# Kernel tuning notes

Measured on AMD Instinct MI355X. Metric: run time of the kernel, lower is better.

The kernel has to match this reference:

```python
import jax, jax.numpy as jnp
import numpy as np

B, T, C, H = 128, 200, 171, 1024  # batch, timesteps, frame_dim, hidden


def setup_inputs() -> dict:
    key = jax.random.key(0)
    ks = jax.random.split(key, 16)
    s = 1.0 / np.sqrt(H)  # PyTorch default init range for LSTMCell/Linear

    def u(k, shape):
        return jax.random.uniform(k, shape, jnp.float32, -s, s)

    inp = {
        "seq": jax.random.normal(ks[0], (B, T, C), jnp.float32),
        # LSTMCell 1: input C -> hidden H
        "W_ih1": u(ks[1], (4 * H, C)), "W_hh1": u(ks[2], (4 * H, H)),
        "b_ih1": u(ks[3], (4 * H,)),   "b_hh1": u(ks[4], (4 * H,)),
        # LSTMCell 2: H -> H
        "W_ih2": u(ks[5], (4 * H, H)), "W_hh2": u(ks[6], (4 * H, H)),
        "b_ih2": u(ks[7], (4 * H,)),   "b_hh2": u(ks[8], (4 * H,)),
        # LSTMCell 3: H -> H
        "W_ih3": u(ks[9], (4 * H, H)), "W_hh3": u(ks[10], (4 * H, H)),
        "b_ih3": u(ks[11], (4 * H,)),  "b_hh3": u(ks[12], (4 * H,)),
        # decoder Linear: H -> C
        "W_dec": u(ks[13], (C, H)), "b_dec": u(ks[14], (C,)),
        "cond": 5, "gt": 5,
    }
    return inp


def _lstm_cell(x, h, c, W_ih, W_hh, b_ih, b_hh):
    # PyTorch LSTMCell gate order: i, f, g, o
    gates = x @ W_ih.T + b_ih + h @ W_hh.T + b_hh
    i, f, g, o = jnp.split(gates, 4, axis=-1)
    c_new = jax.nn.sigmoid(f) * c + jax.nn.sigmoid(i) * jnp.tanh(g)
    h_new = jax.nn.sigmoid(o) * jnp.tanh(c_new)
    return h_new, c_new


def reference(seq, W_ih1, W_hh1, b_ih1, b_hh1,
              W_ih2, W_hh2, b_ih2, b_hh2,
              W_ih3, W_hh3, b_ih3, b_hh3,
              W_dec, b_dec, cond, gt):
    Bb, Tt, Cc = seq.shape
    Hh = W_hh1.shape[1]
    # Static teacher-forcing pattern: gt ground-truth steps, then cond self-conditioned steps.
    pattern = jnp.asarray(np.array(([True] * gt + [False] * cond) * 100, dtype=bool)[:Tt])

    def step(carry, xs):
        h1, c1, h2, c2, h3, c3, xo = carry
        x_t, use_gt = xs
        x = jnp.where(use_gt, x_t, xo)
        h1, c1 = _lstm_cell(x, h1, c1, W_ih1, W_hh1, b_ih1, b_hh1)
        h2, c2 = _lstm_cell(h1, h2, c2, W_ih2, W_hh2, b_ih2, b_hh2)
        h3, c3 = _lstm_cell(h2, h3, c3, W_ih3, W_hh3, b_ih3, b_hh3)
        xo = h3 @ W_dec.T + b_dec
        return (h1, c1, h2, c2, h3, c3, xo), xo

    z = jnp.zeros((Bb, Hh), seq.dtype)
    init = (z, z, z, z, z, z, jnp.zeros((Bb, Cc), seq.dtype))
    _, out = jax.lax.scan(step, init, (seq.transpose(1, 0, 2), pattern))
    return out.transpose(1, 0, 2)  # [B, T, C]
```

## Files before the change

kernel.cpp:

```cpp
#include <hip/hip_runtime.h>

#define TT 200
#define BB 128
#define CC 171
#define HH 1024

typedef __attribute__((ext_vector_type(8))) short short8;
typedef __attribute__((ext_vector_type(4))) float f32x4;

__device__ __forceinline__ unsigned short f2bf(float f) {
  unsigned int u = __float_as_uint(f);
  u += 0x7fff + ((u >> 16) & 1);
  return (unsigned short)(u >> 16);
}
__device__ __forceinline__ float sigmoidf_(float x) { return 1.f / (1.f + __expf(-x)); }

__device__ __forceinline__ int4 ld_coh16(const void* p) {
  int4 r;
  asm volatile("global_load_dwordx4 %0, %1, off sc0 sc1" : "=v"(r) : "v"(p));
  return r;
}
__device__ __forceinline__ void st_coh2(void* p, unsigned int v) {
  asm volatile("global_store_short %0, %1, off sc0 sc1" :: "v"(p), "v"(v) : "memory");
}
__device__ __forceinline__ void drain_vm() {
  asm volatile("s_waitcnt vmcnt(0)" ::: "memory");
}
__device__ __forceinline__ void wait4() {
  asm volatile("s_waitcnt vmcnt(4)" ::: "memory");
}
__device__ __forceinline__ void bar_lds() {
  asm volatile("s_waitcnt lgkmcnt(0)" ::: "memory");
  __builtin_amdgcn_s_barrier();
  asm volatile("" ::: "memory");
}

__device__ __forceinline__ void groupbar(int* B, int tid, int epoch) {
  __builtin_amdgcn_s_barrier();
  if (tid == 0) {
    if (__hip_atomic_fetch_add(&B[0], 1, __ATOMIC_RELAXED, __HIP_MEMORY_SCOPE_AGENT) == epoch * 64 - 1)
      __hip_atomic_store(&B[32], epoch, __ATOMIC_RELAXED, __HIP_MEMORY_SCOPE_AGENT);
    while (__hip_atomic_load(&B[32], __ATOMIC_RELAXED, __HIP_MEMORY_SCOPE_AGENT) < epoch)
      __builtin_amdgcn_s_sleep(1);
  }
  asm volatile("" ::: "memory");
  __builtin_amdgcn_s_barrier();
  asm volatile("" ::: "memory");
}

struct Pre4 { int4 v[4]; };
struct Pre5 { int4 v[5]; };

__device__ __forceinline__ void prefetch_old(const unsigned short* A2, int sA2,
    int m0, int grp, int row, int lj, Pre4& P) {
  const unsigned short* base = A2 + (size_t)(m0 + row) * sA2 + ((lj ^ (row & 7)) << 3);
#pragma unroll
  for (int j = 0; j < 4; ++j)
    P.v[j] = ld_coh16(base + (grp * 4 + j) * 64);
}

__device__ __forceinline__ void prefetch_gtl1(const float* seqt,
    const unsigned short* H1old, int m0, int grp, int row, int lj, Pre5& P) {
  const int kt0 = grp * 5;
  const int ktn = 4 + (grp < 3 ? 1 : 0);
  const float* srow = seqt + (size_t)(m0 + row) * (TT * CC);
  const unsigned short* hbase = H1old + (size_t)(m0 + row) * HH + ((lj ^ (row & 7)) << 3);
#pragma unroll
  for (int i = 0; i < 5; ++i) {
    if (i < ktn) {
      int kt = kt0 + i;
      if (kt < 3) {
        int c0 = kt * 64 + ((lj ^ (row & 7)) << 3);
        unsigned int w[4];
#pragma unroll
        for (int jj = 0; jj < 4; ++jj) {
          int ca = c0 + 2 * jj, cb = c0 + 2 * jj + 1;
          float va = (ca < CC) ? srow[ca] : 0.f;
          float vb = (cb < CC) ? srow[cb] : 0.f;
          w[jj] = (unsigned int)f2bf(va) | ((unsigned int)f2bf(vb) << 16);
        }
        P.v[i] = make_int4(w[0], w[1], w[2], w[3]);
      } else {
        P.v[i] = ld_coh16(hbase + (kt - 3) * 64);
      }
    }
  }
  drain_vm();
}

__device__ __forceinline__ void exchange_cell(f32x4 acc0, f32x4 acc1,
    const float* bias, float& creg, unsigned short* Hout,
    char* smem, int m0, int n0, int ntile, int tid) {
  const int wave = tid >> 6, lane = tid & 63;
  const int grp = wave >> 2, gw = wave & 3;
  const int fl = lane & 15, fh = lane >> 4;
  bar_lds();
  float* ex = (float*)smem;
#pragma unroll
  for (int r = 0; r < 4; ++r) {
    ex[((grp * 4 + gw) * 32 + fh * 4 + r) * 16 + fl] = acc0[r];
    ex[((grp * 4 + gw) * 32 + 16 + fh * 4 + r) * 16 + fl] = acc1[r];
  }
  bar_lds();
  if (tid < 512) {
    int urow = tid >> 4, uu = tid & 15;
    float g4[4];
#pragma unroll
    for (int gg = 0; gg < 4; ++gg) {
      float s = ex[(gg * 32 + urow) * 16 + uu] + ex[((4 + gg) * 32 + urow) * 16 + uu]
              + ex[((8 + gg) * 32 + urow) * 16 + uu] + ex[((12 + gg) * 32 + urow) * 16 + uu];
      g4[gg] = s + bias[n0 + gg * 16 + uu];
    }
    float cn = sigmoidf_(g4[1]) * creg + sigmoidf_(g4[0]) * tanhf(g4[2]);
    creg = cn;
    st_coh2(Hout + (size_t)(m0 + urow) * HH + ntile * 16 + uu,
            (unsigned int)f2bf(sigmoidf_(g4[3]) * tanhf(cn)));
  }
}

__device__ __forceinline__ void lstm_split(
    const unsigned short* __restrict__ A1, int sA1,
    const unsigned short* __restrict__ Wa, int sWa,
    const unsigned short* __restrict__ Wb, int sWb,
    const float* __restrict__ bias,
    float& creg, unsigned short* __restrict__ Hout,
    char* smem, int m0, int n0, int ntile, int tid, const Pre4& P)
{
  const int wave = tid >> 6, lane = tid & 63;
  const int grp = wave >> 2, gw = wave & 3;
  const int lrow = lane >> 3, lj = lane & 7;
  const int fl = lane & 15, fh = lane >> 4;
  const int row = gw * 8 + lrow;
  const int swz = (fl & 7) << 4;
  const int wrowi = n0 + gw * 16 + fl;
  char* G = smem + grp * 32768;

  int4 anew[4];
  const unsigned short* nbase = A1 + (size_t)(m0 + row) * sA1 + ((lj ^ (row & 7)) << 3);
#pragma unroll
  for (int j = 0; j < 4; ++j)
    anew[j] = ld_coh16(nbase + (grp * 4 + j) * 64);
  wait4();
#pragma unroll
  for (int j = 0; j < 4; ++j)
    *(int4*)(G + (4 + j) * 4096 + row * 128 + lj * 16) = P.v[j];
  bar_lds();

  f32x4 acc0 = {0.f, 0.f, 0.f, 0.f}, acc1 = {0.f, 0.f, 0.f, 0.f};
  const unsigned short* wbr = Wb + (size_t)wrowi * sWb + fh * 8;
#pragma unroll
  for (int j = 0; j < 4; ++j) {
#pragma unroll
    for (int kk = 0; kk < 2; ++kk) {
      short8 b0 = *(const short8*)(wbr + (grp * 4 + j) * 64 + kk * 32);
      int colb = kk * 64 + fh * 16;
      short8 a0 = *(const short8*)(G + (4 + j) * 4096 + fl * 128 + (colb ^ swz));
      short8 a1 = *(const short8*)(G + (4 + j) * 4096 + (16 + fl) * 128 + (colb ^ swz));
      acc0 = __builtin_amdgcn_mfma_f32_16x16x32_bf16(a0, b0, acc0, 0, 0, 0);
      acc1 = __builtin_amdgcn_mfma_f32_16x16x32_bf16(a1, b0, acc1, 0, 0, 0);
    }
  }
  drain_vm();
#pragma unroll
  for (int j = 0; j < 4; ++j)
    *(int4*)(G + j * 4096 + row * 128 + lj * 16) = anew[j];
  bar_lds();
  const unsigned short* war = Wa + (size_t)wrowi * sWa + fh * 8;
#pragma unroll
  for (int j = 0; j < 4; ++j) {
#pragma unroll
    for (int kk = 0; kk < 2; ++kk) {
      short8 b0 = *(const short8*)(war + (grp * 4 + j) * 64 + kk * 32);
      int colb = kk * 64 + fh * 16;
      short8 a0 = *(const short8*)(G + j * 4096 + fl * 128 + (colb ^ swz));
      short8 a1 = *(const short8*)(G + j * 4096 + (16 + fl) * 128 + (colb ^ swz));
      acc0 = __builtin_amdgcn_mfma_f32_16x16x32_bf16(a0, b0, acc0, 0, 0, 0);
      acc1 = __builtin_amdgcn_mfma_f32_16x16x32_bf16(a1, b0, acc1, 0, 0, 0);
    }
  }
  exchange_cell(acc0, acc1, bias, creg, Hout, smem, m0, n0, ntile, tid);
}

__device__ __forceinline__ void lstm_gtl1(const Pre5& P,
    const unsigned short* __restrict__ Wih1p, const unsigned short* __restrict__ Whh1,
    const float* __restrict__ bias,
    float& creg, unsigned short* __restrict__ Hout,
    char* smem, int m0, int n0, int ntile, int tid)
{
  const int wave = tid >> 6, lane = tid & 63;
  const int grp = wave >> 2, gw = wave & 3;
  const int lrow = lane >> 3, lj = lane & 7;
  const int fl = lane & 15, fh = lane >> 4;
  const int row = gw * 8 + lrow;
  const int swz = (fl & 7) << 4;
  const int wrowi = n0 + gw * 16 + fl;
  const int kt0 = grp * 5;
  const int ktn = 4 + (grp < 3 ? 1 : 0);
  char* G = smem + grp * 32768;

#pragma unroll
  for (int i = 0; i < 5; ++i)
    if (i < ktn) *(int4*)(G + i * 4096 + row * 128 + lj * 16) = P.v[i];
  bar_lds();

  f32x4 acc0 = {0.f, 0.f, 0.f, 0.f}, acc1 = {0.f, 0.f, 0.f, 0.f};
#pragma unroll
  for (int i = 0; i < 5; ++i) {
    if (i < ktn) {
      int kt = kt0 + i;
      const unsigned short* wr = (kt < 3)
          ? Wih1p + (size_t)wrowi * 192 + kt * 64 + fh * 8
          : Whh1 + (size_t)wrowi * HH + (kt - 3) * 64 + fh * 8;
#pragma unroll
      for (int kk = 0; kk < 2; ++kk) {
        short8 b0 = *(const short8*)(wr + kk * 32);
        int colb = kk * 64 + fh * 16;
        short8 a0 = *(const short8*)(G + i * 4096 + fl * 128 + (colb ^ swz));
        short8 a1 = *(const short8*)(G + i * 4096 + (16 + fl) * 128 + (colb ^ swz));
        acc0 = __builtin_amdgcn_mfma_f32_16x16x32_bf16(a0, b0, acc0, 0, 0, 0);
        acc1 = __builtin_amdgcn_mfma_f32_16x16x32_bf16(a1, b0, acc1, 0, 0, 0);
      }
    }
  }
  exchange_cell(acc0, acc1, bias, creg, Hout, smem, m0, n0, ntile, tid);
}

__device__ __forceinline__ void dec_out(
    const unsigned short* __restrict__ H3in, const unsigned short* __restrict__ Wd,
    const float* __restrict__ bd, float* __restrict__ out,
    int t, char* smem, int d, int tid, int m0)
{
  const int wave = tid >> 6, lane = tid & 63;
  const int lrow = lane >> 3, lj = lane & 7;
  const int fl = lane & 15, fh = lane >> 4;
  const int n0 = d * 16;
  char* Dr = smem + 65536 + wave * 4096;
  int4 r4[4];
#pragma unroll
  for (int j = 0; j < 4; ++j) {
    int row = j * 8 + lrow;
    r4[j] = ld_coh16(H3in + (size_t)(m0 + row) * HH + wave * 64 + ((lj ^ (row & 7)) << 3));
  }
  drain_vm();
#pragma unroll
  for (int j = 0; j < 4; ++j) {
    int row = j * 8 + lrow;
    *(int4*)(Dr + row * 128 + lj * 16) = r4[j];
  }
  f32x4 acc0 = {0.f, 0.f, 0.f, 0.f}, acc1 = {0.f, 0.f, 0.f, 0.f};
  const unsigned short* Wrow = Wd + (size_t)(n0 + fl) * HH + wave * 64 + fh * 8;
  const int swz = (fl & 7) << 4;
#pragma unroll
  for (int kk = 0; kk < 2; ++kk) {
    short8 b0 = *(const short8*)(Wrow + kk * 32);
    int colb = kk * 64 + fh * 16;
    short8 a0 = *(const short8*)(Dr + fl * 128 + (colb ^ swz));
    short8 a1 = *(const short8*)(Dr + (16 + fl) * 128 + (colb ^ swz));
    acc0 = __builtin_amdgcn_mfma_f32_16x16x32_bf16(a0, b0, acc0, 0, 0, 0);
    acc1 = __builtin_amdgcn_mfma_f32_16x16x32_bf16(a1, b0, acc1, 0, 0, 0);
  }
  float* pex = (float*)(smem + 32768);
#pragma unroll
  for (int r = 0; r < 4; ++r) {
    pex[(wave * 32 + fh * 4 + r) * 16 + fl] = acc0[r];
    pex[(wave * 32 + 16 + fh * 4 + r) * 16 + fl] = acc1[r];
  }
  bar_lds();
  if (tid < 512) {
    int rrow = tid >> 4, uu = tid & 15;
    int c = n0 + uu;
    if (c < CC) {
      float s = 0.f;
#pragma unroll
      for (int v = 0; v < 16; ++v) s += pex[(v * 32 + rrow) * 16 + uu];
      out[(size_t)(m0 + rrow) * (TT * CC) + (size_t)t * CC + c] = s + bd[c];
    }
  }
}

__global__ __launch_bounds__(1024, 4) void persistent_lstm(
    const unsigned short* __restrict__ Wih1p, const unsigned short* __restrict__ Whh1,
    const unsigned short* __restrict__ Wf, const unsigned short* __restrict__ W2,
    const unsigned short* __restrict__ W3, const unsigned short* __restrict__ Wd,
    const float* __restrict__ B1gt, const float* __restrict__ B1sc,
    const float* __restrict__ B2, const float* __restrict__ B3, const float* __restrict__ Bd,
    unsigned short* __restrict__ Hb, const float* __restrict__ seq, float* __restrict__ out,
    const int* __restrict__ gtp, const int* __restrict__ condp, int* __restrict__ bar)
{
  __shared__ char smem[131072];
  const int wg = blockIdx.x, tid = threadIdx.x;
  const int xg = wg & 7, sl = wg >> 3;
  const int ntile = xg * 8 + (sl >> 2);
  const int mgrp = sl & 3;
  const int m0 = mgrp * 32;
  const int n0 = ntile * 64;
  const int gt = *gtp, cond = *condp;
  const int per = gt + cond;
  const int lane = tid & 63, wave = tid >> 6;
  const int grp = wave >> 2, gw = wave & 3;
  const int lrow = lane >> 3, lj = lane & 7;
  const int row = gw * 8 + lrow;

  int dd = ((ntile & 7) << 3) | (ntile >> 3);
  const int decid = (dd < 11) ? dd : -1;

  unsigned short* H1[2] = { Hb + 0 * BB * HH, Hb + 1 * BB * HH };
  unsigned short* H2[2] = { Hb + 2 * BB * HH, Hb + 3 * BB * HH };
  unsigned short* H3[2] = { Hb + 4 * BB * HH, Hb + 5 * BB * HH };
  int* B = bar + mgrp * 256;

  float c1 = 0.f, c2 = 0.f, c3 = 0.f;
  Pre4 aold; Pre5 a1pre;
  int e = 0, tm = 0;
  bool gts = (per > 0) ? (0 < gt) : true;
  if (gts) prefetch_gtl1(seq, H1[0], m0, grp, row, lj, a1pre);
  else     prefetch_old(H1[0], HH, m0, grp, row, lj, aold);

  for (int t = 0; t < TT; ++t) {
    int p = t & 1;
    if (gts) lstm_gtl1(a1pre, Wih1p, Whh1, B1gt, c1, H1[1 - p], smem, m0, n0, ntile, tid);
    else     lstm_split(H3[p], HH, Wf, HH, Whh1, HH, B1sc, c1, H1[1 - p],
                        smem, m0, n0, ntile, tid, aold);
    if (decid >= 0 && t > 0) dec_out(H3[p], Wd, Bd, out, t - 1, smem, decid, tid, m0);
    prefetch_old(H2[p], HH, m0, grp, row, lj, aold);
    wait4();
    groupbar(B, tid, ++e);
    lstm_split(H1[1 - p], HH, W2, 2048, W2 + 1024, 2048, B2, c2, H2[1 - p],
               smem, m0, n0, ntile, tid, aold);
    prefetch_old(H3[p], HH, m0, grp, row, lj, aold);
    wait4();
    groupbar(B, tid, ++e);
    lstm_split(H2[1 - p], HH, W3, 2048, W3 + 1024, 2048, B3, c3, H3[1 - p],
               smem, m0, n0, ntile, tid, aold);
    int tmn = (tm + 1 == per) ? 0 : tm + 1;
    bool gtsn = (per > 0) ? (tmn < gt) : true;
    if (t + 1 < TT) {
      if (gtsn) prefetch_gtl1(seq + (size_t)(t + 1) * CC, H1[1 - p], m0, grp, row, lj, a1pre);
      else { prefetch_old(H1[1 - p], HH, m0, grp, row, lj, aold); wait4(); }
    } else drain_vm();
    groupbar(B, tid, ++e);
    tm = tmn; gts = gtsn;
  }
  if (decid >= 0) dec_out(H3[0], Wd, Bd, out, TT - 1, smem, decid, tid, m0);
}

__device__ __forceinline__ int perm_orig_row(int np) {
  return ((np >> 4) & 3) * HH + ((np >> 6) << 4) + (np & 15);
}

__global__ void conv_wih1p(const float* __restrict__ Wih, unsigned short* __restrict__ dst) {
  int np = blockIdx.x, k = threadIdx.x;
  int n = perm_orig_row(np);
  dst[(size_t)np * 192 + k] = f2bf((k < CC) ? Wih[(size_t)n * CC + k] : 0.f);
}

__global__ void conv_whh1(const float* __restrict__ Whh, unsigned short* __restrict__ dst) {
  int np = blockIdx.y, k = blockIdx.x * 256 + threadIdx.x;
  int n = perm_orig_row(np);
  dst[(size_t)np * HH + k] = f2bf(Whh[(size_t)n * HH + k]);
}

__global__ void conv_w23(const float* __restrict__ Wih, const float* __restrict__ Whh,
                         unsigned short* __restrict__ dst) {
  int k = blockIdx.x * 256 + threadIdx.x;
  int np = blockIdx.y;
  int n = perm_orig_row(np);
  float v = (k < HH) ? Wih[(size_t)n * HH + k] : Whh[(size_t)n * HH + (k - HH)];
  dst[(size_t)np * 2048 + k] = f2bf(v);
}

__global__ void conv_wd(const float* __restrict__ Wsrc, unsigned short* __restrict__ dst) {
  int k = blockIdx.x * 256 + threadIdx.x;
  int row = blockIdx.y;
  dst[(size_t)row * HH + k] = f2bf((row < CC) ? Wsrc[(size_t)row * HH + k] : 0.f);
}

__global__ void wf_gemm(const float* __restrict__ Wih1, const float* __restrict__ Wdec,
                        unsigned short* __restrict__ Wfo) {
  int j = blockIdx.x * 256 + threadIdx.x;
  int np = blockIdx.y;
  int n = perm_orig_row(np);
  const float* wr = Wih1 + (size_t)n * CC;
  float acc = 0.f;
  for (int c = 0; c < CC; ++c) acc = fmaf(wr[c], Wdec[(size_t)c * HH + j], acc);
  Wfo[(size_t)np * HH + j] = f2bf(acc);
}

__global__ void bias_all(const float* bi1, const float* bh1, const float* Wih1, const float* bdec,
                         const float* bi2, const float* bh2, const float* bi3, const float* bh3,
                         float* o1gt, float* o1sc, float* o2, float* o3, float* od) {
  int idx = blockIdx.x * 256 + threadIdx.x;
  if (idx < 4096) {
    int n = perm_orig_row(idx);
    float b = bi1[n] + bh1[n];
    o1gt[idx] = b;
    const float* wr = Wih1 + (size_t)n * CC;
    float acc = 0.f;
    for (int c = 0; c < CC; ++c) acc = fmaf(wr[c], bdec[c], acc);
    o1sc[idx] = b + acc;
  } else if (idx < 8192) {
    int np = idx - 4096; int n = perm_orig_row(np);
    o2[np] = bi2[n] + bh2[n];
  } else if (idx < 12288) {
    int np = idx - 8192; int n = perm_orig_row(np);
    o3[np] = bi3[n] + bh3[n];
  } else if (idx < 12464) {
    int c2 = idx - 12288;
    od[c2] = (c2 < CC) ? bdec[c2] : 0.f;
  }
}

__global__ void init_state(unsigned short* __restrict__ Hall, int* __restrict__ bar) {
  int idx = blockIdx.x * blockDim.x + threadIdx.x;
  if (idx < 6 * BB * HH) Hall[idx] = 0;
  if (idx < 1024) bar[idx] = 0;
}

extern "C" void kernel_launch(void* const* d_in, const int* in_sizes, int n_in,
                              void* d_out, int out_size, void* d_ws, size_t ws_size,
                              hipStream_t stream)
{
  const float* seq   = (const float*)d_in[0];
  const float* W_ih1 = (const float*)d_in[1];
  const float* W_hh1 = (const float*)d_in[2];
  const float* b_ih1 = (const float*)d_in[3];
  const float* b_hh1 = (const float*)d_in[4];
  const float* W_ih2 = (const float*)d_in[5];
  const float* W_hh2 = (const float*)d_in[6];
  const float* b_ih2 = (const float*)d_in[7];
  const float* b_hh2 = (const float*)d_in[8];
  const float* W_ih3 = (const float*)d_in[9];
  const float* W_hh3 = (const float*)d_in[10];
  const float* b_ih3 = (const float*)d_in[11];
  const float* b_hh3 = (const float*)d_in[12];
  const float* W_dec = (const float*)d_in[13];
  const float* b_dec = (const float*)d_in[14];
  const int* condp   = (const int*)d_in[15];
  const int* gtp     = (const int*)d_in[16];
  float* out = (float*)d_out;
  char* ws = (char*)d_ws;

  if (ws_size < 53908480) return;

  unsigned short* Wih1p = (unsigned short*)(ws + 0);
  unsigned short* Whh1  = (unsigned short*)(ws + 1572864);
  unsigned short* Wf    = (unsigned short*)(ws + 9961472);
  unsigned short* W2    = (unsigned short*)(ws + 18350080);
  unsigned short* W3    = (unsigned short*)(ws + 35127296);
  unsigned short* Wd    = (unsigned short*)(ws + 51904512);
  float* B1gt = (float*)(ws + 52264960);
  float* B1sc = (float*)(ws + 52281344);
  float* B2   = (float*)(ws + 52297728);
  float* B3   = (float*)(ws + 52314112);
  float* Bd   = (float*)(ws + 52330496);
  unsigned short* Hbase = (unsigned short*)(ws + 52331520);
  int* bar = (int*)(ws + 53904384);

  conv_wih1p<<<dim3(4096),    192, 0, stream>>>(W_ih1, Wih1p);
  conv_whh1 <<<dim3(4, 4096), 256, 0, stream>>>(W_hh1, Whh1);
  wf_gemm   <<<dim3(4, 4096), 256, 0, stream>>>(W_ih1, W_dec, Wf);
  conv_w23  <<<dim3(8, 4096), 256, 0, stream>>>(W_ih2, W_hh2, W2);
  conv_w23  <<<dim3(8, 4096), 256, 0, stream>>>(W_ih3, W_hh3, W3);
  conv_wd   <<<dim3(4, 176),  256, 0, stream>>>(W_dec, Wd);
  bias_all  <<<dim3(49),      256, 0, stream>>>(b_ih1, b_hh1, W_ih1, b_dec,
                                                b_ih2, b_hh2, b_ih3, b_hh3,
                                                B1gt, B1sc, B2, B3, Bd);
  init_state<<<dim3(3072),    256, 0, stream>>>(Hbase, bar);

  persistent_lstm<<<dim3(256), dim3(1024), 0, stream>>>(
      Wih1p, Whh1, Wf, W2, W3, Wd, B1gt, B1sc, B2, B3, Bd,
      Hbase, seq, out, gtp, condp, bar);
}
```

Baseline: 7.139 ms.

## Split persistent LSTM into 512 workgroups of 512 threads with 16-row batch tiles

The persistent kernel moves from 256 workgroups of 1024 threads (32 batch rows each) to 512 workgroups of 512 threads (16 batch rows each). Each wave now computes two 16-column N tiles that share one A fragment, so A is read from LDS once per pair of MFMAs. LDS per workgroup halves, and the group barrier now spans 8 batch groups of 64 workgroups each. The intent is better occupancy and spread across CUs, at the cost of twice as many workgroups reloading the weights, more barrier instances, and a reworked decoder split over 8 waves.

```diff
diff --git a/kernel.cpp b/kernel.cpp
--- a/kernel.cpp
+++ b/kernel.cpp
@@ -26,7 +26,7 @@
 __device__ __forceinline__ void drain_vm() {
   asm volatile("s_waitcnt vmcnt(0)" ::: "memory");
 }
-__device__ __forceinline__ void wait4() {
+__device__ __forceinline__ void waitN4() {
   asm volatile("s_waitcnt vmcnt(4)" ::: "memory");
 }
 __device__ __forceinline__ void bar_lds() {
@@ -51,32 +51,33 @@
 struct Pre4 { int4 v[4]; };
 struct Pre5 { int4 v[5]; };
 
-__device__ __forceinline__ void prefetch_old(const unsigned short* A2, int sA2,
-    int m0, int grp, int row, int lj, Pre4& P) {
-  const unsigned short* base = A2 + (size_t)(m0 + row) * sA2 + ((lj ^ (row & 7)) << 3);
+
+__device__ __forceinline__ void prefetch_old(const unsigned short* A2, int m0,
+                                             int grp, int srow, int cj, Pre4& P) {
+  const unsigned short* base = A2 + (size_t)(m0 + srow) * HH + ((cj ^ (srow & 7)) << 3);
 #pragma unroll
   for (int j = 0; j < 4; ++j)
     P.v[j] = ld_coh16(base + (grp * 4 + j) * 64);
 }
 
-__device__ __forceinline__ void prefetch_gtl1(const float* seqt,
-    const unsigned short* H1old, int m0, int grp, int row, int lj, Pre5& P) {
+__device__ __forceinline__ void prefetch_gtl1(const float* seqt, const unsigned short* H1old,
+                                              int m0, int grp, int srow, int cj, Pre5& P) {
   const int kt0 = grp * 5;
   const int ktn = 4 + (grp < 3 ? 1 : 0);
-  const float* srow = seqt + (size_t)(m0 + row) * (TT * CC);
-  const unsigned short* hbase = H1old + (size_t)(m0 + row) * HH + ((lj ^ (row & 7)) << 3);
+  const float* srowp = seqt + (size_t)(m0 + srow) * (TT * CC);
+  const unsigned short* hbase = H1old + (size_t)(m0 + srow) * HH + ((cj ^ (srow & 7)) << 3);
 #pragma unroll
   for (int i = 0; i < 5; ++i) {
     if (i < ktn) {
       int kt = kt0 + i;
       if (kt < 3) {
-        int c0 = kt * 64 + ((lj ^ (row & 7)) << 3);
+        int c0 = kt * 64 + ((cj ^ (srow & 7)) << 3);
         unsigned int w[4];
 #pragma unroll
         for (int jj = 0; jj < 4; ++jj) {
           int ca = c0 + 2 * jj, cb = c0 + 2 * jj + 1;
-          float va = (ca < CC) ? srow[ca] : 0.f;
-          float vb = (cb < CC) ? srow[cb] : 0.f;
+          float va = (ca < CC) ? srowp[ca] : 0.f;
+          float vb = (cb < CC) ? srowp[cb] : 0.f;
           w[jj] = (unsigned int)f2bf(va) | ((unsigned int)f2bf(vb) << 16);
         }
         P.v[i] = make_int4(w[0], w[1], w[2], w[3]);
@@ -92,23 +93,23 @@
     const float* bias, float& creg, unsigned short* Hout,
     char* smem, int m0, int n0, int ntile, int tid) {
   const int wave = tid >> 6, lane = tid & 63;
-  const int grp = wave >> 2, gw = wave & 3;
+  const int grp = wave >> 1, gw = wave & 1;
   const int fl = lane & 15, fh = lane >> 4;
   bar_lds();
   float* ex = (float*)smem;
 #pragma unroll
   for (int r = 0; r < 4; ++r) {
-    ex[((grp * 4 + gw) * 32 + fh * 4 + r) * 16 + fl] = acc0[r];
-    ex[((grp * 4 + gw) * 32 + 16 + fh * 4 + r) * 16 + fl] = acc1[r];
-  }
-  bar_lds();
-  if (tid < 512) {
+    ex[((grp * 4 + gw * 2 + 0) * 16 + fh * 4 + r) * 16 + fl] = acc0[r];
+    ex[((grp * 4 + gw * 2 + 1) * 16 + fh * 4 + r) * 16 + fl] = acc1[r];
+  }
+  bar_lds();
+  if (tid < 256) {
     int urow = tid >> 4, uu = tid & 15;
     float g4[4];
 #pragma unroll
     for (int gg = 0; gg < 4; ++gg) {
-      float s = ex[(gg * 32 + urow) * 16 + uu] + ex[((4 + gg) * 32 + urow) * 16 + uu]
-              + ex[((8 + gg) * 32 + urow) * 16 + uu] + ex[((12 + gg) * 32 + urow) * 16 + uu];
+      float s = ex[((0 + gg) * 16 + urow) * 16 + uu] + ex[((4 + gg) * 16 + urow) * 16 + uu]
+              + ex[((8 + gg) * 16 + urow) * 16 + uu] + ex[((12 + gg) * 16 + urow) * 16 + uu];
       g4[gg] = s + bias[n0 + gg * 16 + uu];
     }
     float cn = sigmoidf_(g4[1]) * creg + sigmoidf_(g4[0]) * tanhf(g4[2]);
@@ -119,7 +120,7 @@
 }
 
 __device__ __forceinline__ void lstm_split(
-    const unsigned short* __restrict__ A1, int sA1,
+    const unsigned short* __restrict__ A1,
     const unsigned short* __restrict__ Wa, int sWa,
     const unsigned short* __restrict__ Wb, int sWb,
     const float* __restrict__ bias,
@@ -127,55 +128,53 @@
     char* smem, int m0, int n0, int ntile, int tid, const Pre4& P)
 {
   const int wave = tid >> 6, lane = tid & 63;
-  const int grp = wave >> 2, gw = wave & 3;
-  const int lrow = lane >> 3, lj = lane & 7;
+  const int grp = wave >> 1, gw = wave & 1;
+  const int srow = gw * 8 + (lane >> 3), cj = lane & 7;
   const int fl = lane & 15, fh = lane >> 4;
-  const int row = gw * 8 + lrow;
   const int swz = (fl & 7) << 4;
-  const int wrowi = n0 + gw * 16 + fl;
-  char* G = smem + grp * 32768;
+  char* G = smem + grp * 16384;
 
   int4 anew[4];
-  const unsigned short* nbase = A1 + (size_t)(m0 + row) * sA1 + ((lj ^ (row & 7)) << 3);
+  const unsigned short* nb = A1 + (size_t)(m0 + srow) * HH + ((cj ^ (srow & 7)) << 3);
 #pragma unroll
   for (int j = 0; j < 4; ++j)
-    anew[j] = ld_coh16(nbase + (grp * 4 + j) * 64);
-  wait4();
+    anew[j] = ld_coh16(nb + (grp * 4 + j) * 64);
+  waitN4();
 #pragma unroll
   for (int j = 0; j < 4; ++j)
-    *(int4*)(G + (4 + j) * 4096 + row * 128 + lj * 16) = P.v[j];
+    *(int4*)(G + (4 + j) * 2048 + srow * 128 + cj * 16) = P.v[j];
   bar_lds();
 
   f32x4 acc0 = {0.f, 0.f, 0.f, 0.f}, acc1 = {0.f, 0.f, 0.f, 0.f};
-  const unsigned short* wbr = Wb + (size_t)wrowi * sWb + fh * 8;
+  const unsigned short* wb0 = Wb + (size_t)(n0 + gw * 32 + fl) * sWb + fh * 8;
+  const unsigned short* wb1 = wb0 + 16 * sWb;
 #pragma unroll
   for (int j = 0; j < 4; ++j) {
 #pragma unroll
     for (int kk = 0; kk < 2; ++kk) {
-      short8 b0 = *(const short8*)(wbr + (grp * 4 + j) * 64 + kk * 32);
-      int colb = kk * 64 + fh * 16;
-      short8 a0 = *(const short8*)(G + (4 + j) * 4096 + fl * 128 + (colb ^ swz));
-      short8 a1 = *(const short8*)(G + (4 + j) * 4096 + (16 + fl) * 128 + (colb ^ swz));
-      acc0 = __builtin_amdgcn_mfma_f32_16x16x32_bf16(a0, b0, acc0, 0, 0, 0);
-      acc1 = __builtin_amdgcn_mfma_f32_16x16x32_bf16(a1, b0, acc1, 0, 0, 0);
+      short8 b0 = *(const short8*)(wb0 + (grp * 4 + j) * 64 + kk * 32);
+      short8 b1 = *(const short8*)(wb1 + (grp * 4 + j) * 64 + kk * 32);
+      short8 a = *(const short8*)(G + (4 + j) * 2048 + fl * 128 + ((kk * 64 + fh * 16) ^ swz));
+      acc0 = __builtin_amdgcn_mfma_f32_16x16x32_bf16(a, b0, acc0, 0, 0, 0);
+      acc1 = __builtin_amdgcn_mfma_f32_16x16x32_bf16(a, b1, acc1, 0, 0, 0);
     }
   }
   drain_vm();
 #pragma unroll
   for (int j = 0; j < 4; ++j)
-    *(int4*)(G + j * 4096 + row * 128 + lj * 16) = anew[j];
-  bar_lds();
-  const unsigned short* war = Wa + (size_t)wrowi * sWa + fh * 8;
+    *(int4*)(G + j * 2048 + srow * 128 + cj * 16) = anew[j];
+  bar_lds();
+  const unsigned short* wa0 = Wa + (size_t)(n0 + gw * 32 + fl) * sWa + fh * 8;
+  const unsigned short* wa1 = wa0 + 16 * sWa;
 #pragma unroll
   for (int j = 0; j < 4; ++j) {
 #pragma unroll
     for (int kk = 0; kk < 2; ++kk) {
-      short8 b0 = *(const short8*)(war + (grp * 4 + j) * 64 + kk * 32);
-      int colb = kk * 64 + fh * 16;
-      short8 a0 = *(const short8*)(G + j * 4096 + fl * 128 + (colb ^ swz));
-      short8 a1 = *(const short8*)(G + j * 4096 + (16 + fl) * 128 + (colb ^ swz));
-      acc0 = __builtin_amdgcn_mfma_f32_16x16x32_bf16(a0, b0, acc0, 0, 0, 0);
-      acc1 = __builtin_amdgcn_mfma_f32_16x16x32_bf16(a1, b0, acc1, 0, 0, 0);
+      short8 b0 = *(const short8*)(wa0 + (grp * 4 + j) * 64 + kk * 32);
+      short8 b1 = *(const short8*)(wa1 + (grp * 4 + j) * 64 + kk * 32);
+      short8 a = *(const short8*)(G + j * 2048 + fl * 128 + ((kk * 64 + fh * 16) ^ swz));
+      acc0 = __builtin_amdgcn_mfma_f32_16x16x32_bf16(a, b0, acc0, 0, 0, 0);
+      acc1 = __builtin_amdgcn_mfma_f32_16x16x32_bf16(a, b1, acc1, 0, 0, 0);
     }
   }
   exchange_cell(acc0, acc1, bias, creg, Hout, smem, m0, n0, ntile, tid);
@@ -188,19 +187,17 @@
     char* smem, int m0, int n0, int ntile, int tid)
 {
   const int wave = tid >> 6, lane = tid & 63;
-  const int grp = wave >> 2, gw = wave & 3;
-  const int lrow = lane >> 3, lj = lane & 7;
+  const int grp = wave >> 1, gw = wave & 1;
+  const int srow = gw * 8 + (lane >> 3), cj = lane & 7;
   const int fl = lane & 15, fh = lane >> 4;
-  const int row = gw * 8 + lrow;
   const int swz = (fl & 7) << 4;
-  const int wrowi = n0 + gw * 16 + fl;
   const int kt0 = grp * 5;
   const int ktn = 4 + (grp < 3 ? 1 : 0);
-  char* G = smem + grp * 32768;
+  char* G = smem + grp * 16384;
 
 #pragma unroll
   for (int i = 0; i < 5; ++i)
-    if (i < ktn) *(int4*)(G + i * 4096 + row * 128 + lj * 16) = P.v[i];
+    if (i < ktn) *(int4*)(G + i * 2048 + srow * 128 + cj * 16) = P.v[i];
   bar_lds();
 
   f32x4 acc0 = {0.f, 0.f, 0.f, 0.f}, acc1 = {0.f, 0.f, 0.f, 0.f};
@@ -208,77 +205,78 @@
   for (int i = 0; i < 5; ++i) {
     if (i < ktn) {
       int kt = kt0 + i;
-      const unsigned short* wr = (kt < 3)
-          ? Wih1p + (size_t)wrowi * 192 + kt * 64 + fh * 8
-          : Whh1 + (size_t)wrowi * HH + (kt - 3) * 64 + fh * 8;
+      int sW = (kt < 3) ? 192 : HH;
+      const unsigned short* wr0 = ((kt < 3)
+          ? Wih1p + (size_t)(n0 + gw * 32 + fl) * 192 + kt * 64
+          : Whh1 + (size_t)(n0 + gw * 32 + fl) * HH + (kt - 3) * 64) + fh * 8;
+      const unsigned short* wr1 = wr0 + 16 * sW;
 #pragma unroll
       for (int kk = 0; kk < 2; ++kk) {
-        short8 b0 = *(const short8*)(wr + kk * 32);
-        int colb = kk * 64 + fh * 16;
-        short8 a0 = *(const short8*)(G + i * 4096 + fl * 128 + (colb ^ swz));
-        short8 a1 = *(const short8*)(G + i * 4096 + (16 + fl) * 128 + (colb ^ swz));
-        acc0 = __builtin_amdgcn_mfma_f32_16x16x32_bf16(a0, b0, acc0, 0, 0, 0);
-        acc1 = __builtin_amdgcn_mfma_f32_16x16x32_bf16(a1, b0, acc1, 0, 0, 0);
+        short8 b0 = *(const short8*)(wr0 + kk * 32);
+        short8 b1 = *(const short8*)(wr1 + kk * 32);
+        short8 a = *(const short8*)(G + i * 2048 + fl * 128 + ((kk * 64 + fh * 16) ^ swz));
+        acc0 = __builtin_amdgcn_mfma_f32_16x16x32_bf16(a, b0, acc0, 0, 0, 0);
+        acc1 = __builtin_amdgcn_mfma_f32_16x16x32_bf16(a, b1, acc1, 0, 0, 0);
       }
     }
   }
   exchange_cell(acc0, acc1, bias, creg, Hout, smem, m0, n0, ntile, tid);
 }
 
-__device__ __forceinline__ void dec_out(
-    const unsigned short* __restrict__ H3in, const unsigned short* __restrict__ Wd,
-    const float* __restrict__ bd, float* __restrict__ out,
-    int t, char* smem, int d, int tid, int m0)
+__device__ __forceinline__ void dec_exec(const unsigned short* __restrict__ H3in,
+    const unsigned short* __restrict__ Wd, const float* __restrict__ bd,
+    float* __restrict__ out, int t, char* smem, int dd, int tid, int m0)
 {
   const int wave = tid >> 6, lane = tid & 63;
-  const int lrow = lane >> 3, lj = lane & 7;
+  const int cj = lane & 7;
   const int fl = lane & 15, fh = lane >> 4;
-  const int n0 = d * 16;
-  char* Dr = smem + 65536 + wave * 4096;
-  int4 r4[4];
-#pragma unroll
-  for (int j = 0; j < 4; ++j) {
-    int row = j * 8 + lrow;
-    r4[j] = ld_coh16(H3in + (size_t)(m0 + row) * HH + wave * 64 + ((lj ^ (row & 7)) << 3));
+  const int swz = (fl & 7) << 4;
+  int4 P[4];
+#pragma unroll
+  for (int q = 0; q < 4; ++q) {
+    int k = q >> 1, s = q & 1;
+    int row = s * 8 + (lane >> 3);
+    P[q] = ld_coh16(H3in + (size_t)(m0 + row) * HH + wave * 128 + k * 64 + ((cj ^ (row & 7)) << 3));
   }
   drain_vm();
-#pragma unroll
-  for (int j = 0; j < 4; ++j) {
-    int row = j * 8 + lrow;
-    *(int4*)(Dr + row * 128 + lj * 16) = r4[j];
-  }
-  f32x4 acc0 = {0.f, 0.f, 0.f, 0.f}, acc1 = {0.f, 0.f, 0.f, 0.f};
-  const unsigned short* Wrow = Wd + (size_t)(n0 + fl) * HH + wave * 64 + fh * 8;
-  const int swz = (fl & 7) << 4;
-#pragma unroll
-  for (int kk = 0; kk < 2; ++kk) {
-    short8 b0 = *(const short8*)(Wrow + kk * 32);
-    int colb = kk * 64 + fh * 16;
-    short8 a0 = *(const short8*)(Dr + fl * 128 + (colb ^ swz));
-    short8 a1 = *(const short8*)(Dr + (16 + fl) * 128 + (colb ^ swz));
-    acc0 = __builtin_amdgcn_mfma_f32_16x16x32_bf16(a0, b0, acc0, 0, 0, 0);
-    acc1 = __builtin_amdgcn_mfma_f32_16x16x32_bf16(a1, b0, acc1, 0, 0, 0);
-  }
-  float* pex = (float*)(smem + 32768);
-#pragma unroll
-  for (int r = 0; r < 4; ++r) {
-    pex[(wave * 32 + fh * 4 + r) * 16 + fl] = acc0[r];
-    pex[(wave * 32 + 16 + fh * 4 + r) * 16 + fl] = acc1[r];
-  }
-  bar_lds();
-  if (tid < 512) {
+  char* Dr = smem + 16384 + wave * 4096;
+#pragma unroll
+  for (int q = 0; q < 4; ++q) {
+    int k = q >> 1, s = q & 1;
+    int row = s * 8 + (lane >> 3);
+    *(int4*)(Dr + k * 2048 + row * 128 + cj * 16) = P[q];
+  }
+  bar_lds();
+  f32x4 acc = {0.f, 0.f, 0.f, 0.f};
+  const unsigned short* wr = Wd + (size_t)(dd * 16 + fl) * HH + wave * 128 + fh * 8;
+#pragma unroll
+  for (int k = 0; k < 2; ++k) {
+#pragma unroll
+    for (int kk = 0; kk < 2; ++kk) {
+      short8 b0 = *(const short8*)(wr + k * 64 + kk * 32);
+      short8 a = *(const short8*)(Dr + k * 2048 + fl * 128 + ((kk * 64 + fh * 16) ^ swz));
+      acc = __builtin_amdgcn_mfma_f32_16x16x32_bf16(a, b0, acc, 0, 0, 0);
+    }
+  }
+  bar_lds();
+  float* pex = (float*)smem;
+#pragma unroll
+  for (int r = 0; r < 4; ++r)
+    pex[(wave * 16 + fh * 4 + r) * 16 + fl] = acc[r];
+  bar_lds();
+  if (tid < 256) {
     int rrow = tid >> 4, uu = tid & 15;
-    int c = n0 + uu;
+    int c = dd * 16 + uu;
     if (c < CC) {
       float s = 0.f;
 #pragma unroll
-      for (int v = 0; v < 16; ++v) s += pex[(v * 32 + rrow) * 16 + uu];
+      for (int v = 0; v < 8; ++v) s += pex[(v * 16 + rrow) * 16 + uu];
       out[(size_t)(m0 + rrow) * (TT * CC) + (size_t)t * CC + c] = s + bd[c];
     }
   }
 }
 
-__global__ __launch_bounds__(1024, 4) void persistent_lstm(
+__global__ __launch_bounds__(512, 4) void persistent_lstm(
     const unsigned short* __restrict__ Wih1p, const unsigned short* __restrict__ Whh1,
     const unsigned short* __restrict__ Wf, const unsigned short* __restrict__ W2,
     const unsigned short* __restrict__ W3, const unsigned short* __restrict__ Wd,
@@ -287,19 +285,19 @@
     unsigned short* __restrict__ Hb, const float* __restrict__ seq, float* __restrict__ out,
     const int* __restrict__ gtp, const int* __restrict__ condp, int* __restrict__ bar)
 {
-  __shared__ char smem[131072];
+  __shared__ char smem[65536];
   const int wg = blockIdx.x, tid = threadIdx.x;
-  const int xg = wg & 7, sl = wg >> 3;
+  const int w8 = wg & 255, half = wg >> 8;
+  const int xg = w8 & 7, sl = w8 >> 3;
+  const int mgrp = (sl & 3) + half * 4;
+  const int m0 = mgrp * 16;
   const int ntile = xg * 8 + (sl >> 2);
-  const int mgrp = sl & 3;
-  const int m0 = mgrp * 32;
   const int n0 = ntile * 64;
   const int gt = *gtp, cond = *condp;
   const int per = gt + cond;
   const int lane = tid & 63, wave = tid >> 6;
-  const int grp = wave >> 2, gw = wave & 3;
-  const int lrow = lane >> 3, lj = lane & 7;
-  const int row = gw * 8 + lrow;
+  const int grp = wave >> 1, gw = wave & 1;
+  const int srow = gw * 8 + (lane >> 3), cj = lane & 7;
 
   int dd = ((ntile & 7) << 3) | (ntile >> 3);
   const int decid = (dd < 11) ? dd : -1;
@@ -307,41 +305,42 @@
   unsigned short* H1[2] = { Hb + 0 * BB * HH, Hb + 1 * BB * HH };
   unsigned short* H2[2] = { Hb + 2 * BB * HH, Hb + 3 * BB * HH };
   unsigned short* H3[2] = { Hb + 4 * BB * HH, Hb + 5 * BB * HH };
-  int* B = bar + mgrp * 256;
+  int* B = bar + mgrp * 64;
 
   float c1 = 0.f, c2 = 0.f, c3 = 0.f;
   Pre4 aold; Pre5 a1pre;
   int e = 0, tm = 0;
   bool gts = (per > 0) ? (0 < gt) : true;
-  if (gts) prefetch_gtl1(seq, H1[0], m0, grp, row, lj, a1pre);
-  else     prefetch_old(H1[0], HH, m0, grp, row, lj, aold);
+  if (gts) prefetch_gtl1(seq, H1[0], m0, grp, srow, cj, a1pre);
+  else   { prefetch_old(H1[0], m0, grp, srow, cj, aold); waitN4(); }
 
   for (int t = 0; t < TT; ++t) {
     int p = t & 1;
     if (gts) lstm_gtl1(a1pre, Wih1p, Whh1, B1gt, c1, H1[1 - p], smem, m0, n0, ntile, tid);
-    else     lstm_split(H3[p], HH, Wf, HH, Whh1, HH, B1sc, c1, H1[1 - p],
+    else     lstm_split(H3[p], Wf, HH, Whh1, HH, B1sc, c1, H1[1 - p],
                         smem, m0, n0, ntile, tid, aold);
-    if (decid >= 0 && t > 0) dec_out(H3[p], Wd, Bd, out, t - 1, smem, decid, tid, m0);
-    prefetch_old(H2[p], HH, m0, grp, row, lj, aold);
-    wait4();
+    if (decid >= 0 && t > 0) dec_exec(H3[p], Wd, Bd, out, t - 1, smem, decid, tid, m0);
+    prefetch_old(H2[p], m0, grp, srow, cj, aold);
+    waitN4();
     groupbar(B, tid, ++e);
-    lstm_split(H1[1 - p], HH, W2, 2048, W2 + 1024, 2048, B2, c2, H2[1 - p],
+    lstm_split(H1[1 - p], W2, 2048, W2 + 1024, 2048, B2, c2, H2[1 - p],
                smem, m0, n0, ntile, tid, aold);
-    prefetch_old(H3[p], HH, m0, grp, row, lj, aold);
-    wait4();
+    prefetch_old(H3[p], m0, grp, srow, cj, aold);
+    waitN4();
     groupbar(B, tid, ++e);
-    lstm_split(H2[1 - p], HH, W3, 2048, W3 + 1024, 2048, B3, c3, H3[1 - p],
+    lstm_split(H2[1 - p], W3, 2048, W3 + 1024, 2048, B3, c3, H3[1 - p],
                smem, m0, n0, ntile, tid, aold);
     int tmn = (tm + 1 == per) ? 0 : tm + 1;
     bool gtsn = (per > 0) ? (tmn < gt) : true;
     if (t + 1 < TT) {
-      if (gtsn) prefetch_gtl1(seq + (size_t)(t + 1) * CC, H1[1 - p], m0, grp, row, lj, a1pre);
-      else { prefetch_old(H1[1 - p], HH, m0, grp, row, lj, aold); wait4(); }
+      if (gtsn) prefetch_gtl1(seq + (size_t)(t + 1) * CC, H1[1 - p], m0, grp, srow, cj, a1pre);
+      else { prefetch_old(H1[1 - p], m0, grp, srow, cj, aold); waitN4(); }
     } else drain_vm();
     groupbar(B, tid, ++e);
     tm = tmn; gts = gtsn;
   }
-  if (decid >= 0) dec_out(H3[0], Wd, Bd, out, TT - 1, smem, decid, tid, m0);
+  if (decid >= 0)
+    dec_exec(H3[0], Wd, Bd, out, TT - 1, smem, decid, tid, m0);
 }
 
 __device__ __forceinline__ int perm_orig_row(int np) {
@@ -467,7 +466,7 @@
                                                 B1gt, B1sc, B2, B3, Bd);
   init_state<<<dim3(3072),    256, 0, stream>>>(Hbase, bar);
 
-  persistent_lstm<<<dim3(256), dim3(1024), 0, stream>>>(
+  persistent_lstm<<<dim3(512), dim3(512), 0, stream>>>(
       Wih1p, Whh1, Wf, W2, W3, Wd, B1gt, B1sc, B2, B3, Bd,
       Hbase, seq, out, gtp, condp, bar);
 }
```

After: 11.85 ms. 66.0% more time.

## Defer decoder output to a post-loop pass using stored h3 history

Applied to the files above, without the earlier changes.

Layer-3 hidden states are now kept for every timestep in a workspace history buffer, but only when the workspace is large enough. The per-step decoder projection is taken off the recurrent critical path and all timesteps are decoded after the loop, spread across all tiles. The group barrier also becomes a single counter polled directly instead of counter plus flag. This trades extra memory traffic and workspace for a shorter serial step; if the workspace is too small, the old ping-pong path is used instead.

```diff
diff --git a/kernel.cpp b/kernel.cpp
--- a/kernel.cpp
+++ b/kernel.cpp
@@ -26,7 +26,7 @@
 __device__ __forceinline__ void drain_vm() {
   asm volatile("s_waitcnt vmcnt(0)" ::: "memory");
 }
-__device__ __forceinline__ void wait4() {
+__device__ __forceinline__ void waitN4() {
   asm volatile("s_waitcnt vmcnt(4)" ::: "memory");
 }
 __device__ __forceinline__ void bar_lds() {
@@ -38,9 +38,8 @@
 __device__ __forceinline__ void groupbar(int* B, int tid, int epoch) {
   __builtin_amdgcn_s_barrier();
   if (tid == 0) {
-    if (__hip_atomic_fetch_add(&B[0], 1, __ATOMIC_RELAXED, __HIP_MEMORY_SCOPE_AGENT) == epoch * 64 - 1)
-      __hip_atomic_store(&B[32], epoch, __ATOMIC_RELAXED, __HIP_MEMORY_SCOPE_AGENT);
-    while (__hip_atomic_load(&B[32], __ATOMIC_RELAXED, __HIP_MEMORY_SCOPE_AGENT) < epoch)
+    __hip_atomic_fetch_add(&B[0], 1, __ATOMIC_RELAXED, __HIP_MEMORY_SCOPE_AGENT);
+    while (__hip_atomic_load(&B[0], __ATOMIC_RELAXED, __HIP_MEMORY_SCOPE_AGENT) < epoch * 64)
       __builtin_amdgcn_s_sleep(1);
   }
   asm volatile("" ::: "memory");
@@ -51,16 +50,17 @@
 struct Pre4 { int4 v[4]; };
 struct Pre5 { int4 v[5]; };
 
-__device__ __forceinline__ void prefetch_old(const unsigned short* A2, int sA2,
-    int m0, int grp, int row, int lj, Pre4& P) {
-  const unsigned short* base = A2 + (size_t)(m0 + row) * sA2 + ((lj ^ (row & 7)) << 3);
+
+__device__ __forceinline__ void prefetch_old(const unsigned short* A2, int m0,
+                                             int grp, int row, int lj, Pre4& P) {
+  const unsigned short* base = A2 + (size_t)(m0 + row) * HH + ((lj ^ (row & 7)) << 3);
 #pragma unroll
   for (int j = 0; j < 4; ++j)
     P.v[j] = ld_coh16(base + (grp * 4 + j) * 64);
 }
 
-__device__ __forceinline__ void prefetch_gtl1(const float* seqt,
-    const unsigned short* H1old, int m0, int grp, int row, int lj, Pre5& P) {
+__device__ __forceinline__ void prefetch_gtl1(const float* seqt, const unsigned short* H1old,
+                                              int m0, int grp, int row, int lj, Pre5& P) {
   const int kt0 = grp * 5;
   const int ktn = 4 + (grp < 3 ? 1 : 0);
   const float* srow = seqt + (size_t)(m0 + row) * (TT * CC);
@@ -107,7 +107,7 @@
     float g4[4];
 #pragma unroll
     for (int gg = 0; gg < 4; ++gg) {
-      float s = ex[(gg * 32 + urow) * 16 + uu] + ex[((4 + gg) * 32 + urow) * 16 + uu]
+      float s = ex[((0 + gg) * 32 + urow) * 16 + uu] + ex[((4 + gg) * 32 + urow) * 16 + uu]
               + ex[((8 + gg) * 32 + urow) * 16 + uu] + ex[((12 + gg) * 32 + urow) * 16 + uu];
       g4[gg] = s + bias[n0 + gg * 16 + uu];
     }
@@ -119,7 +119,7 @@
 }
 
 __device__ __forceinline__ void lstm_split(
-    const unsigned short* __restrict__ A1, int sA1,
+    const unsigned short* __restrict__ A1,
     const unsigned short* __restrict__ Wa, int sWa,
     const unsigned short* __restrict__ Wb, int sWb,
     const float* __restrict__ bias,
@@ -132,22 +132,21 @@
   const int fl = lane & 15, fh = lane >> 4;
   const int row = gw * 8 + lrow;
   const int swz = (fl & 7) << 4;
-  const int wrowi = n0 + gw * 16 + fl;
   char* G = smem + grp * 32768;
 
   int4 anew[4];
-  const unsigned short* nbase = A1 + (size_t)(m0 + row) * sA1 + ((lj ^ (row & 7)) << 3);
+  const unsigned short* nb = A1 + (size_t)(m0 + row) * HH + ((lj ^ (row & 7)) << 3);
 #pragma unroll
   for (int j = 0; j < 4; ++j)
-    anew[j] = ld_coh16(nbase + (grp * 4 + j) * 64);
-  wait4();
+    anew[j] = ld_coh16(nb + (grp * 4 + j) * 64);
+  waitN4();
 #pragma unroll
   for (int j = 0; j < 4; ++j)
     *(int4*)(G + (4 + j) * 4096 + row * 128 + lj * 16) = P.v[j];
   bar_lds();
 
   f32x4 acc0 = {0.f, 0.f, 0.f, 0.f}, acc1 = {0.f, 0.f, 0.f, 0.f};
-  const unsigned short* wbr = Wb + (size_t)wrowi * sWb + fh * 8;
+  const unsigned short* wbr = Wb + (size_t)(n0 + gw * 16 + fl) * sWb + fh * 8;
 #pragma unroll
   for (int j = 0; j < 4; ++j) {
 #pragma unroll
@@ -165,7 +164,7 @@
   for (int j = 0; j < 4; ++j)
     *(int4*)(G + j * 4096 + row * 128 + lj * 16) = anew[j];
   bar_lds();
-  const unsigned short* war = Wa + (size_t)wrowi * sWa + fh * 8;
+  const unsigned short* war = Wa + (size_t)(n0 + gw * 16 + fl) * sWa + fh * 8;
 #pragma unroll
   for (int j = 0; j < 4; ++j) {
 #pragma unroll
@@ -193,7 +192,6 @@
   const int fl = lane & 15, fh = lane >> 4;
   const int row = gw * 8 + lrow;
   const int swz = (fl & 7) << 4;
-  const int wrowi = n0 + gw * 16 + fl;
   const int kt0 = grp * 5;
   const int ktn = 4 + (grp < 3 ? 1 : 0);
   char* G = smem + grp * 32768;
@@ -209,8 +207,8 @@
     if (i < ktn) {
       int kt = kt0 + i;
       const unsigned short* wr = (kt < 3)
-          ? Wih1p + (size_t)wrowi * 192 + kt * 64 + fh * 8
-          : Whh1 + (size_t)wrowi * HH + (kt - 3) * 64 + fh * 8;
+          ? Wih1p + (size_t)(n0 + gw * 16 + fl) * 192 + kt * 64 + fh * 8
+          : Whh1 + (size_t)(n0 + gw * 16 + fl) * HH + (kt - 3) * 64 + fh * 8;
 #pragma unroll
       for (int kk = 0; kk < 2; ++kk) {
         short8 b0 = *(const short8*)(wr + kk * 32);
@@ -247,6 +245,7 @@
     int row = j * 8 + lrow;
     *(int4*)(Dr + row * 128 + lj * 16) = r4[j];
   }
+  bar_lds();
   f32x4 acc0 = {0.f, 0.f, 0.f, 0.f}, acc1 = {0.f, 0.f, 0.f, 0.f};
   const unsigned short* Wrow = Wd + (size_t)(n0 + fl) * HH + wave * 64 + fh * 8;
   const int swz = (fl & 7) << 4;
@@ -276,15 +275,18 @@
       out[(size_t)(m0 + rrow) * (TT * CC) + (size_t)t * CC + c] = s + bd[c];
     }
   }
-}
-
-__global__ __launch_bounds__(1024, 4) void persistent_lstm(
+  bar_lds();
+}
+
+template<bool HIST>
+__global__ __launch_bounds__(1024, 1) void persistent_lstm(
     const unsigned short* __restrict__ Wih1p, const unsigned short* __restrict__ Whh1,
     const unsigned short* __restrict__ Wf, const unsigned short* __restrict__ W2,
     const unsigned short* __restrict__ W3, const unsigned short* __restrict__ Wd,
     const float* __restrict__ B1gt, const float* __restrict__ B1sc,
     const float* __restrict__ B2, const float* __restrict__ B3, const float* __restrict__ Bd,
-    unsigned short* __restrict__ Hb, const float* __restrict__ seq, float* __restrict__ out,
+    unsigned short* __restrict__ Hb, unsigned short* __restrict__ H3s,
+    const float* __restrict__ seq, float* __restrict__ out,
     const int* __restrict__ gtp, const int* __restrict__ condp, int* __restrict__ bar)
 {
   __shared__ char smem[131072];
@@ -298,50 +300,60 @@
   const int per = gt + cond;
   const int lane = tid & 63, wave = tid >> 6;
   const int grp = wave >> 2, gw = wave & 3;
-  const int lrow = lane >> 3, lj = lane & 7;
-  const int row = gw * 8 + lrow;
+  const int row = gw * 8 + (lane >> 3), lj = lane & 7;
 
   int dd = ((ntile & 7) << 3) | (ntile >> 3);
   const int decid = (dd < 11) ? dd : -1;
 
   unsigned short* H1[2] = { Hb + 0 * BB * HH, Hb + 1 * BB * HH };
   unsigned short* H2[2] = { Hb + 2 * BB * HH, Hb + 3 * BB * HH };
-  unsigned short* H3[2] = { Hb + 4 * BB * HH, Hb + 5 * BB * HH };
-  int* B = bar + mgrp * 256;
+  int* B = bar + mgrp * 64;
 
   float c1 = 0.f, c2 = 0.f, c3 = 0.f;
   Pre4 aold; Pre5 a1pre;
   int e = 0, tm = 0;
   bool gts = (per > 0) ? (0 < gt) : true;
   if (gts) prefetch_gtl1(seq, H1[0], m0, grp, row, lj, a1pre);
-  else     prefetch_old(H1[0], HH, m0, grp, row, lj, aold);
+  else   { prefetch_old(H3s , m0, grp, row, lj, aold); waitN4(); }
+  if (!gts) { prefetch_old(H1[0], m0, grp, row, lj, aold); waitN4(); }
 
   for (int t = 0; t < TT; ++t) {
     int p = t & 1;
+    const unsigned short* h3prev = H3s + (size_t)(HIST ? t : (t & 1)) * (BB * HH);
+    unsigned short* h3out = H3s + (size_t)(HIST ? (t + 1) : ((t + 1) & 1)) * (BB * HH);
     if (gts) lstm_gtl1(a1pre, Wih1p, Whh1, B1gt, c1, H1[1 - p], smem, m0, n0, ntile, tid);
-    else     lstm_split(H3[p], HH, Wf, HH, Whh1, HH, B1sc, c1, H1[1 - p],
+    else     lstm_split(h3prev, Wf, HH, Whh1, HH, B1sc, c1, H1[1 - p],
                         smem, m0, n0, ntile, tid, aold);
-    if (decid >= 0 && t > 0) dec_out(H3[p], Wd, Bd, out, t - 1, smem, decid, tid, m0);
-    prefetch_old(H2[p], HH, m0, grp, row, lj, aold);
-    wait4();
+    if (!HIST && decid >= 0 && t > 0)
+      dec_out(h3prev, Wd, Bd, out, t - 1, smem, decid, tid, m0);
+    prefetch_old(H2[p], m0, grp, row, lj, aold);
+    waitN4();
     groupbar(B, tid, ++e);
-    lstm_split(H1[1 - p], HH, W2, 2048, W2 + 1024, 2048, B2, c2, H2[1 - p],
+    lstm_split(H1[1 - p], W2, 2048, W2 + 1024, 2048, B2, c2, H2[1 - p],
                smem, m0, n0, ntile, tid, aold);
-    prefetch_old(H3[p], HH, m0, grp, row, lj, aold);
-    wait4();
+    prefetch_old(h3prev, m0, grp, row, lj, aold);
+    waitN4();
     groupbar(B, tid, ++e);
-    lstm_split(H2[1 - p], HH, W3, 2048, W3 + 1024, 2048, B3, c3, H3[1 - p],
+    lstm_split(H2[1 - p], W3, 2048, W3 + 1024, 2048, B3, c3, h3out,
                smem, m0, n0, ntile, tid, aold);
     int tmn = (tm + 1 == per) ? 0 : tm + 1;
     bool gtsn = (per > 0) ? (tmn < gt) : true;
     if (t + 1 < TT) {
       if (gtsn) prefetch_gtl1(seq + (size_t)(t + 1) * CC, H1[1 - p], m0, grp, row, lj, a1pre);
-      else { prefetch_old(H1[1 - p], HH, m0, grp, row, lj, aold); wait4(); }
+      else { prefetch_old(H1[1 - p], m0, grp, row, lj, aold); waitN4(); }
     } else drain_vm();
     groupbar(B, tid, ++e);
     tm = tmn; gts = gtsn;
   }
-  if (decid >= 0) dec_out(H3[0], Wd, Bd, out, TT - 1, smem, decid, tid, m0);
+
+  if (HIST) {
+    for (int j = ntile; j < TT * 11; j += 64) {
+      int t = j / 11, ct = j - t * 11;
+      dec_out(H3s + (size_t)(t + 1) * (BB * HH), Wd, Bd, out, t, smem, ct, tid, m0);
+    }
+  } else if (decid >= 0) {
+    dec_out(H3s + (size_t)(TT & 1) * (BB * HH), Wd, Bd, out, TT - 1, smem, decid, tid, m0);
+  }
 }
 
 __device__ __forceinline__ int perm_orig_row(int np) {
@@ -410,9 +422,10 @@
   }
 }
 
-__global__ void init_state(unsigned short* __restrict__ Hall, int* __restrict__ bar) {
+__global__ void init_state(unsigned short* __restrict__ Hall, int nelem,
+                           int* __restrict__ bar) {
   int idx = blockIdx.x * blockDim.x + threadIdx.x;
-  if (idx < 6 * BB * HH) Hall[idx] = 0;
+  if (idx < nelem) Hall[idx] = 0;
   if (idx < 1024) bar[idx] = 0;
 }
 
@@ -440,7 +453,13 @@
   float* out = (float*)d_out;
   char* ws = (char*)d_ws;
 
-  if (ws_size < 53908480) return;
+  const size_t SLOT = (size_t)BB * HH * 2;
+  const size_t HBOFF = 52331520;
+  const size_t H3OFF = HBOFF + 4 * SLOT;
+  const size_t needHist = H3OFF + 201 * SLOT + 4096;
+  const size_t needPing = H3OFF + 2 * SLOT + 4096;
+  if (ws_size < needPing) return;
+  const bool hist = (ws_size >= needHist);
 
   unsigned short* Wih1p = (unsigned short*)(ws + 0);
   unsigned short* Whh1  = (unsigned short*)(ws + 1572864);
@@ -453,8 +472,9 @@
   float* B2   = (float*)(ws + 52297728);
   float* B3   = (float*)(ws + 52314112);
   float* Bd   = (float*)(ws + 52330496);
-  unsigned short* Hbase = (unsigned short*)(ws + 52331520);
-  int* bar = (int*)(ws + 53904384);
+  unsigned short* Hb  = (unsigned short*)(ws + HBOFF);
+  unsigned short* H3s = (unsigned short*)(ws + H3OFF);
+  int* bar = (int*)(ws + H3OFF + (hist ? 201 : 2) * SLOT);
 
   conv_wih1p<<<dim3(4096),    192, 0, stream>>>(W_ih1, Wih1p);
   conv_whh1 <<<dim3(4, 4096), 256, 0, stream>>>(W_hh1, Whh1);
@@ -465,9 +485,14 @@
   bias_all  <<<dim3(49),      256, 0, stream>>>(b_ih1, b_hh1, W_ih1, b_dec,
                                                 b_ih2, b_hh2, b_ih3, b_hh3,
                                                 B1gt, B1sc, B2, B3, Bd);
-  init_state<<<dim3(3072),    256, 0, stream>>>(Hbase, bar);
-
-  persistent_lstm<<<dim3(256), dim3(1024), 0, stream>>>(
-      Wih1p, Whh1, Wf, W2, W3, Wd, B1gt, B1sc, B2, B3, Bd,
-      Hbase, seq, out, gtp, condp, bar);
-}
+  init_state<<<dim3(3072), 256, 0, stream>>>(Hb, (hist ? 5 : 6) * BB * HH, bar);
+
+  if (hist)
+    persistent_lstm<true><<<dim3(256), dim3(1024), 0, stream>>>(
+        Wih1p, Whh1, Wf, W2, W3, Wd, B1gt, B1sc, B2, B3, Bd,
+        Hb, H3s, seq, out, gtp, condp, bar);
+  else
+    persistent_lstm<false><<<dim3(256), dim3(1024), 0, stream>>>(
+        Wih1p, Whh1, Wf, W2, W3, Wd, B1gt, B1sc, B2, B3, Bd,
+        Hb, H3s, seq, out, gtp, condp, bar);
+}
```

New measurement: 6.761 ms. -5.3%, faster.
